# Kernel optimization log

Hardware: AMD Instinct MI355X
Metric: run time of the kernel (lower is better)

## Reference

```python
import jax, jax.numpy as jnp
import numpy as np

B, L, K1, P = 16, 224, 8192, 16  # batch, spectral bands, pixels, endmembers
LEAKY_SLOPE = 0.01  # torch nn.LeakyReLU default


def setup_inputs() -> dict:
    key = jax.random.key(0)
    ks = jax.random.split(key, 7)
    return {
        "a": jax.random.normal(ks[0], (B, P, K1), jnp.float32),
        "d2": jax.random.normal(ks[1], (B, P, K1), jnp.float32),
        "y": jax.random.normal(ks[2], (B, L, K1), jnp.float32),
        "w3_w": jax.random.normal(ks[3], (P, P), jnp.float32) * 0.1,  # Conv1d(P,P,1) weight squeezed
        "b3_w": jax.random.normal(ks[4], (P, P), jnp.float32) * 0.1,
        "w3_c": jax.random.normal(ks[5], (1, L, P), jnp.float32),     # kernel codebook
        "sigma": jnp.ones((1,), jnp.float32) * 2.0,
        "ca_w": jax.random.normal(ks[6], (2, P), jnp.float32) * 0.1,  # CA Conv1d(P,2,1) weight squeezed
    }


def reference(a, d2, y, w3_w, b3_w, w3_c, sigma, ca_w):
    # h2 = Conv1d(P,P,1)(a - d2)  -> pointwise matmul over channel dim
    h2 = jnp.einsum('pq,bqn->bpn', w3_w, a - d2)  # (B,P,K1)

    # GaussianKernelLayer: pairwise L2 distances between y pixels (B,L,K1)
    # and codebook columns w3_c (1,L,P), via the GEMM identity
    # ||u-v||^2 = ||u||^2 + ||v||^2 - 2 u.v  (avoids the (B,L,K1,P) broadcast).
    y_sq = jnp.sum(y * y, axis=1)            # (B,K1)
    c_sq = jnp.sum(w3_c * w3_c, axis=1)      # (1,P)
    cross = jnp.einsum('blk,olp->bkp', y, w3_c)  # (B,K1,P)
    dist_sq = jnp.maximum(y_sq[:, :, None] + c_sq[:, None, :] - 2.0 * cross, 0.0)
    dist = jnp.sqrt(dist_sq)                 # (B,K1,P)
    h3 = jnp.exp(-0.5 * jnp.square(dist / sigma[0]))
    h3 = jnp.transpose(h3, (0, 2, 1))        # (B,P,K1)

    # CA channel attention: avg/max pool over pixels -> Conv1d(P,2,1) -> LeakyReLU -> softmax
    avg = jnp.mean(h3, axis=-1)              # (B,P)
    mx = jnp.max(h3, axis=-1)                # (B,P)
    conv_lrelu = lambda v: jax.nn.leaky_relu(jnp.einsum('cp,bp->bc', ca_w, v), LEAKY_SLOPE)
    ratio = jax.nn.softmax(conv_lrelu(avg) + conv_lrelu(mx), axis=-1)  # (B,2)

    # combine center pixel + mean pixel via bmm with ratio
    mid = h3[:, :, K1 // 2]                  # (B,P)
    mean = jnp.mean(h3, axis=-1)             # (B,P)
    stacked = jnp.stack([mid, mean], axis=1)  # (B,2,P)
    comb = jnp.einsum('bc,bcp->bp', ratio, stacked)  # (B,P)

    # h4 = Conv1d(P,P,1)(comb[:, :, None])
    h4 = jnp.einsum('pq,bq->bp', b3_w, comb)[:, :, None]  # (B,P,1)

    return h4 + h2  # broadcast over pixel dim -> (B,P,K1)
```

## Files before the change

kernel.cpp:

```cpp
#include <hip/hip_runtime.h>

#define Bn  16
#define Ln  224
#define K1n 8192
#define Pn  16
#define NCHUNK 16


__device__ __forceinline__ float readlane_f(float v, int lane) {
    return __uint_as_float(__builtin_amdgcn_readlane(__float_as_uint(v), lane));
}

__global__ __launch_bounds__(256, 1) void k_stats(
    const float* __restrict__ y,
    const float* __restrict__ w3c,
    const float* __restrict__ sigma,
    float* __restrict__ ws_sum,
    float* __restrict__ ws_max,
    float* __restrict__ ws_mid)
{
    __shared__ float s_csq_part[16][Pn];
    __shared__ float s_csq[Pn];
    __shared__ float s_part_s[4][Pn];
    __shared__ float s_part_m[4][Pn];

    const int tid   = threadIdx.x;
    const int lane  = tid & 63;
    const int wv    = tid >> 6;
    const int b     = blockIdx.x >> 4;
    const int chunk = blockIdx.x & 15;

    {
        const int p   = tid & 15;
        const int sub = tid >> 4;
        float cs = 0.f;
#pragma unroll
        for (int l = sub; l < Ln; l += 16) {
            float v = w3c[l * Pn + p];
            cs = fmaf(v, v, cs);
        }
        s_csq_part[sub][p] = cs;
    }
    __syncthreads();
    if (tid < Pn) {
        float cs = 0.f;
#pragma unroll
        for (int s = 0; s < 16; ++s) cs += s_csq_part[s][tid];
        s_csq[tid] = cs;
    }
    __syncthreads();

    float cross0[Pn], cross1[Pn];
#pragma unroll
    for (int p = 0; p < Pn; ++p) { cross0[p] = 0.f; cross1[p] = 0.f; }
    float ysq0 = 0.f, ysq1 = 0.f;

    const float2* yp2 = reinterpret_cast<const float2*>(
                            y + (size_t)b * Ln * K1n + (chunk << 9)) + tid;

    float2 v[8], vn[8];
    float wqa = w3c[lane], wqb = w3c[64 + lane], wqan, wqbn;
#pragma unroll
    for (int j = 0; j < 8; ++j) v[j] = yp2[(size_t)j * (K1n / 2)];

    for (int g = 0; g < Ln / 8; ++g) {
        if (g < Ln / 8 - 1) {
            wqan = w3c[(g + 1) * 128 + lane];
            wqbn = w3c[(g + 1) * 128 + 64 + lane];
#pragma unroll
            for (int j = 0; j < 8; ++j)
                vn[j] = yp2[(size_t)((g + 1) * 8 + j) * (K1n / 2)];
        }
#pragma unroll
        for (int j = 0; j < 8; ++j) {
            const float wreg = (j < 4) ? wqa : wqb;
            ysq0 = fmaf(v[j].x, v[j].x, ysq0);
            ysq1 = fmaf(v[j].y, v[j].y, ysq1);
#pragma unroll
            for (int p = 0; p < Pn; ++p) {
                float w = readlane_f(wreg, (j & 3) * 16 + p);
                cross0[p] = fmaf(v[j].x, w, cross0[p]);
                cross1[p] = fmaf(v[j].y, w, cross1[p]);
            }
        }
        wqa = wqan; wqb = wqbn;
#pragma unroll
        for (int j = 0; j < 8; ++j) v[j] = vn[j];
    }

    const float sg = sigma[0];
    const float nh = -0.5f / (sg * sg);

    float h3e[Pn], h3o[Pn];
#pragma unroll
    for (int p = 0; p < Pn; ++p) {
        float de = fmaxf(ysq0 + s_csq[p] - 2.f * cross0[p], 0.f);
        float dd = fmaxf(ysq1 + s_csq[p] - 2.f * cross1[p], 0.f);
        h3e[p] = __expf(de * nh);
        h3o[p] = __expf(dd * nh);
    }

    if (chunk == 8 && tid == 0) {
#pragma unroll
        for (int p = 0; p < Pn; ++p) ws_mid[b * Pn + p] = h3e[p];
    }

#pragma unroll
    for (int p = 0; p < Pn; ++p) {
        float s = h3e[p] + h3o[p];
        float m = fmaxf(h3e[p], h3o[p]);
#pragma unroll
        for (int off = 32; off > 0; off >>= 1) {
            s += __shfl_down(s, off, 64);
            m = fmaxf(m, __shfl_down(m, off, 64));
        }
        if (lane == 0) { s_part_s[wv][p] = s; s_part_m[wv][p] = m; }
    }
    __syncthreads();
    if (tid < Pn) {
        float s = s_part_s[0][tid] + s_part_s[1][tid] + s_part_s[2][tid] + s_part_s[3][tid];
        float m = fmaxf(fmaxf(s_part_m[0][tid], s_part_m[1][tid]),
                        fmaxf(s_part_m[2][tid], s_part_m[3][tid]));
        const int base = (b * NCHUNK + chunk) * Pn + tid;
        ws_sum[base] = s;
        ws_max[base] = m;
    }
}

__global__ __launch_bounds__(256, 1) void k_out(
    const float* __restrict__ a,
    const float* __restrict__ d2,
    const float* __restrict__ w3w,
    const float* __restrict__ b3w,
    const float* __restrict__ caw,
    const float* __restrict__ ws_sum,
    const float* __restrict__ ws_max,
    const float* __restrict__ ws_mid,
    float* __restrict__ out)
{
    __shared__ float s_w3w[Pn][Pn];
    __shared__ float s_red_s[16][Pn];
    __shared__ float s_red_m[16][Pn];
    __shared__ float s_avg[Pn], s_mx[Pn], s_mid[Pn], s_comb[Pn], s_h4[Pn];
    __shared__ float s_t[2];

    const int tid = threadIdx.x;
    const int b   = blockIdx.x >> 4;
    const int kb  = (blockIdx.x & 15) << 9;

    if (tid < Pn * Pn) s_w3w[tid >> 4][tid & 15] = w3w[tid];

    {
        const int p   = tid & 15;
        const int grp = tid >> 4;
        const int i0  = (b * NCHUNK + grp) * Pn + p;
        s_red_s[grp][p] = ws_sum[i0];
        s_red_m[grp][p] = ws_max[i0];
    }
    __syncthreads();
    if (tid < Pn) {
        float s = 0.f, m = -1.f;
#pragma unroll
        for (int g = 0; g < 16; ++g) {
            s += s_red_s[g][tid];
            m = fmaxf(m, s_red_m[g][tid]);
        }
        s_avg[tid] = s * (1.f / (float)K1n);
        s_mx[tid]  = m;
        s_mid[tid] = ws_mid[b * Pn + tid];
    }
    __syncthreads();

    if (tid < 2) {
        float t1 = 0.f, t2 = 0.f;
        for (int p = 0; p < Pn; ++p) {
            float cw = caw[tid * Pn + p];
            t1 = fmaf(cw, s_avg[p], t1);
            t2 = fmaf(cw, s_mx[p],  t2);
        }
        t1 = (t1 > 0.f) ? t1 : 0.01f * t1;
        t2 = (t2 > 0.f) ? t2 : 0.01f * t2;
        s_t[tid] = t1 + t2;
    }
    __syncthreads();

    if (tid < Pn) {
        float t0 = s_t[0], u1 = s_t[1];
        float mt = fmaxf(t0, u1);
        float e0 = __expf(t0 - mt), e1 = __expf(u1 - mt);
        float inv = 1.f / (e0 + e1);
        s_comb[tid] = (e0 * inv) * s_mid[tid] + (e1 * inv) * s_avg[tid];
    }
    __syncthreads();

    if (tid < Pn) {
        float h = 0.f;
        for (int q = 0; q < Pn; ++q) h = fmaf(b3w[tid * Pn + q], s_comb[q], h);
        s_h4[tid] = h;
    }
    __syncthreads();

    const float2* a2 = reinterpret_cast<const float2*>(
                           a  + (size_t)b * Pn * K1n + kb) + tid;
    const float2* d22 = reinterpret_cast<const float2*>(
                           d2 + (size_t)b * Pn * K1n + kb) + tid;
    float2* o2 = reinterpret_cast<float2*>(
                           out + (size_t)b * Pn * K1n + kb) + tid;

    float2 av[Pn], dv[Pn];
#pragma unroll
    for (int q = 0; q < Pn; ++q) av[q] = a2 [(size_t)q * (K1n / 2)];
#pragma unroll
    for (int q = 0; q < Pn; ++q) dv[q] = d22[(size_t)q * (K1n / 2)];

    float2 diff[Pn];
#pragma unroll
    for (int q = 0; q < Pn; ++q) {
        diff[q].x = av[q].x - dv[q].x;
        diff[q].y = av[q].y - dv[q].y;
    }
#pragma unroll
    for (int p = 0; p < Pn; ++p) {
        float2 h2;
        h2.x = h2.y = s_h4[p];
#pragma unroll
        for (int q = 0; q < Pn; ++q) {
            const float w = s_w3w[p][q];
            h2.x = fmaf(w, diff[q].x, h2.x);
            h2.y = fmaf(w, diff[q].y, h2.y);
        }
        o2[(size_t)p * (K1n / 2)] = h2;
    }
}

extern "C" void kernel_launch(void* const* d_in, const int* in_sizes, int n_in,
                              void* d_out, int out_size, void* d_ws, size_t ws_size,
                              hipStream_t stream) {
    const float* a     = (const float*)d_in[0];
    const float* d2    = (const float*)d_in[1];
    const float* y     = (const float*)d_in[2];
    const float* w3w   = (const float*)d_in[3];
    const float* b3w   = (const float*)d_in[4];
    const float* w3c   = (const float*)d_in[5];
    const float* sigma = (const float*)d_in[6];
    const float* caw   = (const float*)d_in[7];

    float* ws_sum = (float*)d_ws;
    float* ws_max = ws_sum + Bn * NCHUNK * Pn;
    float* ws_mid = ws_max + Bn * NCHUNK * Pn;

    k_stats<<<dim3(Bn * NCHUNK), dim3(256), 0, stream>>>(
        y, w3c, sigma, ws_sum, ws_max, ws_mid);

    k_out<<<dim3(Bn * NCHUNK), dim3(256), 0, stream>>>(
        a, d2, w3w, b3w, caw, ws_sum, ws_max, ws_mid, (float*)d_out);
}
```

Before: 208.7 us.

## Use 512-thread blocks with one pixel per thread and uniform weight loads

Both kernels move from 256 threads handling two pixels each to 512 threads handling one pixel each, with launch bounds allowing two blocks per CU. In k_stats, the readlane-based broadcast of codebook weights is replaced by wave-uniform loads of w3c (scalar loads), and the loop processes 16 bands per group. In k_out, the a/d2 loads are issued before the reduction prologue so memory latency overlaps the attention math, and the w3w shared-memory staging is replaced by direct uniform loads. The aim is more waves in flight to hide memory latency; the cost is loss of float2 vectorization and a larger register footprint per pixel group.

```diff
diff --git a/kernel.cpp b/kernel.cpp
--- a/kernel.cpp
+++ b/kernel.cpp
@@ -5,13 +5,11 @@
 #define K1n 8192
 #define Pn  16
 #define NCHUNK 16
-
-
-__device__ __forceinline__ float readlane_f(float v, int lane) {
-    return __uint_as_float(__builtin_amdgcn_readlane(__float_as_uint(v), lane));
-}
-
-__global__ __launch_bounds__(256, 1) void k_stats(
+#define RG  16
+#define NG  (Ln / RG)
+
+
+__global__ __launch_bounds__(512, 2) void k_stats(
     const float* __restrict__ y,
     const float* __restrict__ w3c,
     const float* __restrict__ sigma,
@@ -19,10 +17,10 @@
     float* __restrict__ ws_max,
     float* __restrict__ ws_mid)
 {
-    __shared__ float s_csq_part[16][Pn];
+    __shared__ float s_csq_part[32][Pn];
     __shared__ float s_csq[Pn];
-    __shared__ float s_part_s[4][Pn];
-    __shared__ float s_part_m[4][Pn];
+    __shared__ float s_part_s[8][Pn];
+    __shared__ float s_part_m[8][Pn];
 
     const int tid   = threadIdx.x;
     const int lane  = tid & 63;
@@ -34,8 +32,7 @@
         const int p   = tid & 15;
         const int sub = tid >> 4;
         float cs = 0.f;
-#pragma unroll
-        for (int l = sub; l < Ln; l += 16) {
+        for (int l = sub; l < Ln; l += 32) {
             float v = w3c[l * Pn + p];
             cs = fmaf(v, v, cs);
         }
@@ -45,70 +42,61 @@
     if (tid < Pn) {
         float cs = 0.f;
 #pragma unroll
-        for (int s = 0; s < 16; ++s) cs += s_csq_part[s][tid];
+        for (int s = 0; s < 32; ++s) cs += s_csq_part[s][tid];
         s_csq[tid] = cs;
     }
     __syncthreads();
 
-    float cross0[Pn], cross1[Pn];
-#pragma unroll
-    for (int p = 0; p < Pn; ++p) { cross0[p] = 0.f; cross1[p] = 0.f; }
-    float ysq0 = 0.f, ysq1 = 0.f;
-
-    const float2* yp2 = reinterpret_cast<const float2*>(
-                            y + (size_t)b * Ln * K1n + (chunk << 9)) + tid;
-
-    float2 v[8], vn[8];
-    float wqa = w3c[lane], wqb = w3c[64 + lane], wqan, wqbn;
-#pragma unroll
-    for (int j = 0; j < 8; ++j) v[j] = yp2[(size_t)j * (K1n / 2)];
-
-    for (int g = 0; g < Ln / 8; ++g) {
-        if (g < Ln / 8 - 1) {
-            wqan = w3c[(g + 1) * 128 + lane];
-            wqbn = w3c[(g + 1) * 128 + 64 + lane];
-#pragma unroll
-            for (int j = 0; j < 8; ++j)
-                vn[j] = yp2[(size_t)((g + 1) * 8 + j) * (K1n / 2)];
-        }
-#pragma unroll
-        for (int j = 0; j < 8; ++j) {
-            const float wreg = (j < 4) ? wqa : wqb;
-            ysq0 = fmaf(v[j].x, v[j].x, ysq0);
-            ysq1 = fmaf(v[j].y, v[j].y, ysq1);
-#pragma unroll
-            for (int p = 0; p < Pn; ++p) {
-                float w = readlane_f(wreg, (j & 3) * 16 + p);
-                cross0[p] = fmaf(v[j].x, w, cross0[p]);
-                cross1[p] = fmaf(v[j].y, w, cross1[p]);
-            }
-        }
-        wqa = wqan; wqb = wqbn;
-#pragma unroll
-        for (int j = 0; j < 8; ++j) v[j] = vn[j];
+    float cross[Pn];
+#pragma unroll
+    for (int p = 0; p < Pn; ++p) cross[p] = 0.f;
+    float ysq = 0.f;
+
+    const float* yp = y + (size_t)b * Ln * K1n + (chunk << 9) + tid;
+
+    float v[RG], vn[RG];
+#pragma unroll
+    for (int j = 0; j < RG; ++j) v[j] = yp[(size_t)j * K1n];
+
+    for (int g = 0; g < NG; ++g) {
+        if (g < NG - 1) {
+#pragma unroll
+            for (int j = 0; j < RG; ++j)
+                vn[j] = yp[(size_t)((g + 1) * RG + j) * K1n];
+        }
+        const float* wrow = w3c + (size_t)g * RG * Pn;
+#pragma unroll
+        for (int j = 0; j < RG; ++j) {
+            ysq = fmaf(v[j], v[j], ysq);
+#pragma unroll
+            for (int p = 0; p < Pn; ++p)
+                cross[p] = fmaf(v[j], wrow[j * Pn + p], cross[p]);
+        }
+        if (g < NG - 1) {
+#pragma unroll
+            for (int j = 0; j < RG; ++j) v[j] = vn[j];
+        }
     }
 
     const float sg = sigma[0];
     const float nh = -0.5f / (sg * sg);
 
-    float h3e[Pn], h3o[Pn];
+    float h3[Pn];
 #pragma unroll
     for (int p = 0; p < Pn; ++p) {
-        float de = fmaxf(ysq0 + s_csq[p] - 2.f * cross0[p], 0.f);
-        float dd = fmaxf(ysq1 + s_csq[p] - 2.f * cross1[p], 0.f);
-        h3e[p] = __expf(de * nh);
-        h3o[p] = __expf(dd * nh);
+        float d = fmaxf(ysq + s_csq[p] - 2.f * cross[p], 0.f);
+        h3[p] = __expf(d * nh);
     }
 
     if (chunk == 8 && tid == 0) {
 #pragma unroll
-        for (int p = 0; p < Pn; ++p) ws_mid[b * Pn + p] = h3e[p];
+        for (int p = 0; p < Pn; ++p) ws_mid[b * Pn + p] = h3[p];
     }
 
 #pragma unroll
     for (int p = 0; p < Pn; ++p) {
-        float s = h3e[p] + h3o[p];
-        float m = fmaxf(h3e[p], h3o[p]);
+        float s = h3[p];
+        float m = h3[p];
 #pragma unroll
         for (int off = 32; off > 0; off >>= 1) {
             s += __shfl_down(s, off, 64);
@@ -118,16 +106,19 @@
     }
     __syncthreads();
     if (tid < Pn) {
-        float s = s_part_s[0][tid] + s_part_s[1][tid] + s_part_s[2][tid] + s_part_s[3][tid];
-        float m = fmaxf(fmaxf(s_part_m[0][tid], s_part_m[1][tid]),
-                        fmaxf(s_part_m[2][tid], s_part_m[3][tid]));
+        float s = 0.f, m = -1.f;
+#pragma unroll
+        for (int w = 0; w < 8; ++w) {
+            s += s_part_s[w][tid];
+            m = fmaxf(m, s_part_m[w][tid]);
+        }
         const int base = (b * NCHUNK + chunk) * Pn + tid;
         ws_sum[base] = s;
         ws_max[base] = m;
     }
 }
 
-__global__ __launch_bounds__(256, 1) void k_out(
+__global__ __launch_bounds__(512, 2) void k_out(
     const float* __restrict__ a,
     const float* __restrict__ d2,
     const float* __restrict__ w3w,
@@ -138,19 +129,24 @@
     const float* __restrict__ ws_mid,
     float* __restrict__ out)
 {
-    __shared__ float s_w3w[Pn][Pn];
     __shared__ float s_red_s[16][Pn];
     __shared__ float s_red_m[16][Pn];
-    __shared__ float s_avg[Pn], s_mx[Pn], s_mid[Pn], s_comb[Pn], s_h4[Pn];
+    __shared__ float s_avg[Pn], s_mx[Pn], s_mid[Pn], s_h4[Pn];
     __shared__ float s_t[2];
 
     const int tid = threadIdx.x;
     const int b   = blockIdx.x >> 4;
     const int kb  = (blockIdx.x & 15) << 9;
 
-    if (tid < Pn * Pn) s_w3w[tid >> 4][tid & 15] = w3w[tid];
-
-    {
+    const float* ap = a  + (size_t)b * Pn * K1n + kb + tid;
+    const float* dp = d2 + (size_t)b * Pn * K1n + kb + tid;
+    float av[Pn], dv[Pn];
+#pragma unroll
+    for (int q = 0; q < Pn; ++q) av[q] = ap[(size_t)q * K1n];
+#pragma unroll
+    for (int q = 0; q < Pn; ++q) dv[q] = dp[(size_t)q * K1n];
+
+    if (tid < 256) {
         const int p   = tid & 15;
         const int grp = tid >> 4;
         const int i0  = (b * NCHUNK + grp) * Pn + p;
@@ -189,47 +185,29 @@
         float mt = fmaxf(t0, u1);
         float e0 = __expf(t0 - mt), e1 = __expf(u1 - mt);
         float inv = 1.f / (e0 + e1);
-        s_comb[tid] = (e0 * inv) * s_mid[tid] + (e1 * inv) * s_avg[tid];
+        s_red_s[0][tid] = (e0 * inv) * s_mid[tid] + (e1 * inv) * s_avg[tid];
     }
     __syncthreads();
 
     if (tid < Pn) {
         float h = 0.f;
-        for (int q = 0; q < Pn; ++q) h = fmaf(b3w[tid * Pn + q], s_comb[q], h);
+        for (int q = 0; q < Pn; ++q) h = fmaf(b3w[tid * Pn + q], s_red_s[0][q], h);
         s_h4[tid] = h;
     }
     __syncthreads();
 
-    const float2* a2 = reinterpret_cast<const float2*>(
-                           a  + (size_t)b * Pn * K1n + kb) + tid;
-    const float2* d22 = reinterpret_cast<const float2*>(
-                           d2 + (size_t)b * Pn * K1n + kb) + tid;
-    float2* o2 = reinterpret_cast<float2*>(
-                           out + (size_t)b * Pn * K1n + kb) + tid;
-
-    float2 av[Pn], dv[Pn];
-#pragma unroll
-    for (int q = 0; q < Pn; ++q) av[q] = a2 [(size_t)q * (K1n / 2)];
-#pragma unroll
-    for (int q = 0; q < Pn; ++q) dv[q] = d22[(size_t)q * (K1n / 2)];
-
-    float2 diff[Pn];
-#pragma unroll
-    for (int q = 0; q < Pn; ++q) {
-        diff[q].x = av[q].x - dv[q].x;
-        diff[q].y = av[q].y - dv[q].y;
-    }
+    float diff[Pn];
+#pragma unroll
+    for (int q = 0; q < Pn; ++q) diff[q] = av[q] - dv[q];
+
+    float* op = out + (size_t)b * Pn * K1n + kb + tid;
 #pragma unroll
     for (int p = 0; p < Pn; ++p) {
-        float2 h2;
-        h2.x = h2.y = s_h4[p];
-#pragma unroll
-        for (int q = 0; q < Pn; ++q) {
-            const float w = s_w3w[p][q];
-            h2.x = fmaf(w, diff[q].x, h2.x);
-            h2.y = fmaf(w, diff[q].y, h2.y);
-        }
-        o2[(size_t)p * (K1n / 2)] = h2;
+        float h2 = s_h4[p];
+#pragma unroll
+        for (int q = 0; q < Pn; ++q)
+            h2 = fmaf(w3w[p * Pn + q], diff[q], h2);
+        op[(size_t)p * K1n] = h2;
     }
 }
 
@@ -249,9 +227,9 @@
     float* ws_max = ws_sum + Bn * NCHUNK * Pn;
     float* ws_mid = ws_max + Bn * NCHUNK * Pn;
 
-    k_stats<<<dim3(Bn * NCHUNK), dim3(256), 0, stream>>>(
+    k_stats<<<dim3(Bn * NCHUNK), dim3(512), 0, stream>>>(
         y, w3c, sigma, ws_sum, ws_max, ws_mid);
 
-    k_out<<<dim3(Bn * NCHUNK), dim3(256), 0, stream>>>(
+    k_out<<<dim3(Bn * NCHUNK), dim3(512), 0, stream>>>(
         a, d2, w3w, b3w, caw, ws_sum, ws_max, ws_mid, (float*)d_out);
 }
```

Result: no change. 211.8 us (+1.5%).
